# Optimization experiments

Measured on AMD Instinct MI355X. Metric: run time of the kernel, lower is better.

## Reference

```python
import jax, jax.numpy as jnp
import numpy as np

N, D = 131072, 64
VOCAB = 1_000_000
N_NEG = 1024
TEMPERATURE = 1.0
EPS = 1e-10
NEG_FILL = -1e9


def setup_inputs() -> dict:
    key = jax.random.key(0)
    k1, k2, k3, k4, k5 = jax.random.split(key, 5)
    hidden = jax.random.normal(k1, (N, D), dtype=jnp.float32)
    y = jax.random.randint(k2, (N,), 0, VOCAB, dtype=jnp.int64)
    sampled_indices = jax.random.randint(k3, (N_NEG,), 0, VOCAB, dtype=jnp.int64)
    emb_table = jax.random.normal(k4, (VOCAB, D), dtype=jnp.float32) * 0.02
    p = jax.random.uniform(k5, (VOCAB,), dtype=jnp.float32) + EPS
    sampling_probs = p / p.sum()  # normalized popularity distribution (buffer)
    return {"hidden": hidden, "y": y, "sampled_indices": sampled_indices,
            "emb_table": emb_table, "sampling_probs": sampling_probs}


def reference(hidden, y, sampled_indices, emb_table, sampling_probs):
    # torch masks rows with y == 0 before the loss; we use weighted mean instead
    # (identical math, jit-friendly static shapes).
    mask = (y != 0).astype(hidden.dtype)                      # [N]
    e_pos = emb_table[y]                                      # [N, D] gather
    e_neg = emb_table[sampled_indices]                        # [K, D] gather
    pos_logits = jnp.einsum('nd,nd->n', hidden, e_pos)        # [N]
    neg_logits = hidden @ e_neg.T                             # [N, K]
    collision = y[:, None] == sampled_indices[None, :]        # [N, K]
    neg_logits = jnp.where(collision, NEG_FILL, neg_logits)
    true_probs = sampling_probs[y]                            # [N]
    sample_probs = sampling_probs[sampled_indices]            # [K]
    pos = pos_logits / TEMPERATURE - jnp.log(true_probs + EPS)        # [N]
    neg = neg_logits / TEMPERATURE - jnp.log(sample_probs + EPS)[None, :]
    logits = jnp.concatenate([pos[:, None], neg], axis=1)     # [N, 1+K]
    # cross-entropy with label 0: logsumexp - logits[:, 0]
    ce = jax.nn.logsumexp(logits, axis=-1) - logits[:, 0]     # [N]
    return jnp.sum(ce * mask) / jnp.maximum(jnp.sum(mask), 1.0)
```

## Files before the change

kernel.cpp:

```cpp
#include <hip/hip_runtime.h>

#define N_ROWS 131072
#define DIM 64
#define KNEG 1024
#define FEPS 1e-10f
#define LOG2E 1.4426950408889634f
#define HSLOTS 2048
#define CPI 128
#define OUTER (KNEG / CPI)
#define CSTR 72

typedef __attribute__((ext_vector_type(8))) short bf16x8;
typedef __attribute__((ext_vector_type(4))) float f32x4;

__device__ __forceinline__ unsigned short f2bf(float x) {
    unsigned int u = __float_as_uint(x);
    unsigned int r = (u + 0x7fffu + ((u >> 16) & 1u)) >> 16;
    return (unsigned short)r;
}

#if __has_builtin(__builtin_amdgcn_exp2f)
__device__ __forceinline__ float fexp2(float x) { return __builtin_amdgcn_exp2f(x); }
#else
__device__ __forceinline__ float fexp2(float x) {
    float r; asm("v_exp_f32 %0, %1\ns_nop 1" : "=v"(r) : "v"(x)); return r;
}
#endif

__device__ __forceinline__ bf16x8 cvt8(float4 u, float4 v) {
    bf16x8 r;
    r[0] = (short)f2bf(u.x * LOG2E); r[1] = (short)f2bf(u.y * LOG2E);
    r[2] = (short)f2bf(u.z * LOG2E); r[3] = (short)f2bf(u.w * LOG2E);
    r[4] = (short)f2bf(v.x * LOG2E); r[5] = (short)f2bf(v.y * LOG2E);
    r[6] = (short)f2bf(v.z * LOG2E); r[7] = (short)f2bf(v.w * LOG2E);
    return r;
}

__global__ __launch_bounds__(1024) void prep_k(
    const float* __restrict__ emb, const int* __restrict__ sidx,
    const float* __restrict__ probs,
    unsigned short* __restrict__ enegPK, float* __restrict__ lf,
    float* __restrict__ gv, int* __restrict__ hkey, float* __restrict__ hval)
{
    const int tid = threadIdx.x;
    if (blockIdx.x < 16) {
        const int gid = blockIdx.x * 1024 + tid;
        const int col = gid >> 4;
        const int j   = gid & 15;
        const int c = sidx[col];
        const float4 v = *(const float4*)(emb + (size_t)c * DIM + j * 4);
        unsigned int lo = (unsigned int)f2bf(v.x) | ((unsigned int)f2bf(v.y) << 16);
        unsigned int hi = (unsigned int)f2bf(v.z) | ((unsigned int)f2bf(v.w) << 16);
        ((uint2*)enegPK)[(size_t)col * 16 + j] = make_uint2(lo, hi);
    } else {
        for (int s = tid; s < HSLOTS; s += 1024) { hkey[s] = -1; hval[s] = 0.0f; }
        const int c = sidx[tid];
        const float L = logf(probs[c] + FEPS);
        __shared__ float red[1024];
        red[tid] = -L;
        __syncthreads();
        for (int s2 = 512; s2 > 0; s2 >>= 1) {
            if (tid < s2) red[tid] = fmaxf(red[tid], red[tid + s2]);
            __syncthreads();
        }
        const float G = red[0] + 2.0f;
        if (tid == 0) gv[0] = G;
        const float lfv = (-L - G) * LOG2E;
        lf[tid] = lfv;
        const float fc = exp2f(lfv);
        unsigned int slot = ((unsigned int)c * 2654435761u) & (HSLOTS - 1);
        for (int it = 0; it < HSLOTS; ++it) {
            int old = atomicCAS(&hkey[slot], -1, c);
            if (old == -1 || old == c) { atomicAdd(&hval[slot], fc); break; }
            slot = (slot + 1) & (HSLOTS - 1);
        }
    }
}

__global__ __launch_bounds__(256, 4) void main_k(
    const float* __restrict__ hidden, const int* __restrict__ y,
    const float* __restrict__ emb, const float* __restrict__ probs,
    const unsigned short* __restrict__ enegPK, const float* __restrict__ lf,
    const float* __restrict__ gv, const int* __restrict__ hkey,
    const float* __restrict__ hval,
    float* __restrict__ pv, float* __restrict__ pw)
{
    __shared__ __align__(16) short bt[2][CPI * CSTR];
    __shared__ float lf_lds[KNEG];

    const int tid  = threadIdx.x;
    const int wid  = tid >> 6;
    const int lane = tid & 63;
    const int quad = lane >> 4;
    const int l15  = lane & 15;

    const int row0 = (blockIdx.x * 4 + wid) * 32;
    const int r0 = row0 + l15;
    const int r1 = row0 + 16 + l15;

    const int y0 = y[r0];
    const int y1 = y[r1];

    for (int i = tid; i < KNEG; i += 256) lf_lds[i] = lf[i];

    const uint4* g4 = (const uint4*)enegPK;
    const int cw = tid >> 3;
    const int ow = tid & 7;
    {
        uint4 u0 = g4[tid], u1 = g4[tid + 256], u2 = g4[tid + 512], u3 = g4[tid + 768];
        short* dst = &bt[0][0];
        *((uint4*)(dst + (cw +  0) * CSTR) + ow) = u0;
        *((uint4*)(dst + (cw + 32) * CSTR) + ow) = u1;
        *((uint4*)(dst + (cw + 64) * CSTR) + ow) = u2;
        *((uint4*)(dst + (cw + 96) * CSTR) + ow) = u3;
    }

    const float* hp0 = hidden + (size_t)r0 * DIM + quad * 8;
    const float* hp1 = hidden + (size_t)r1 * DIM + quad * 8;
    const float4 a0 = *(const float4*)(hp0 + 0);
    const float4 a1 = *(const float4*)(hp0 + 4);
    const float4 a2 = *(const float4*)(hp0 + 32);
    const float4 a3 = *(const float4*)(hp0 + 36);
    const float4 c0 = *(const float4*)(hp1 + 0);
    const float4 c1 = *(const float4*)(hp1 + 4);
    const float4 c2 = *(const float4*)(hp1 + 32);
    const float4 c3 = *(const float4*)(hp1 + 36);

    const float* pe0 = emb + (size_t)y0 * DIM + quad * 8;
    const float* pe1 = emb + (size_t)y1 * DIM + quad * 8;
    const float4 e0 = *(const float4*)(pe0 + 0);
    const float4 e1 = *(const float4*)(pe0 + 4);
    const float4 e2 = *(const float4*)(pe0 + 32);
    const float4 e3 = *(const float4*)(pe0 + 36);
    const float4 g0 = *(const float4*)(pe1 + 0);
    const float4 g1 = *(const float4*)(pe1 + 4);
    const float4 g2 = *(const float4*)(pe1 + 32);
    const float4 g3 = *(const float4*)(pe1 + 36);
    float pd0 = a0.x*e0.x + a0.y*e0.y + a0.z*e0.z + a0.w*e0.w
              + a1.x*e1.x + a1.y*e1.y + a1.z*e1.z + a1.w*e1.w
              + a2.x*e2.x + a2.y*e2.y + a2.z*e2.z + a2.w*e2.w
              + a3.x*e3.x + a3.y*e3.y + a3.z*e3.z + a3.w*e3.w;
    float pd1 = c0.x*g0.x + c0.y*g0.y + c0.z*g0.z + c0.w*g0.w
              + c1.x*g1.x + c1.y*g1.y + c1.z*g1.z + c1.w*g1.w
              + c2.x*g2.x + c2.y*g2.y + c2.z*g2.z + c2.w*g2.w
              + c3.x*g3.x + c3.y*g3.y + c3.z*g3.z + c3.w*g3.w;
    pd0 += __shfl_xor(pd0, 16, 64); pd0 += __shfl_xor(pd0, 32, 64);
    pd1 += __shfl_xor(pd1, 16, 64); pd1 += __shfl_xor(pd1, 32, 64);

    const bf16x8 h00 = cvt8(a0, a1), h01 = cvt8(a2, a3);
    const bf16x8 h10 = cvt8(c0, c1), h11 = cvt8(c2, c3);

    __syncthreads();

    float s00 = 0.f, s01 = 0.f, s02 = 0.f, s03 = 0.f;
    float s10 = 0.f, s11 = 0.f, s12 = 0.f, s13 = 0.f;
    int p = 0;

    for (int t = 0; t < OUTER; ++t) {
        uint4 u0, u1, u2, u3;
        const bool has = (t + 1 < OUTER);
        if (has) {
            const uint4* gs = g4 + (t + 1) * 1024;
            u0 = gs[tid]; u1 = gs[tid + 256]; u2 = gs[tid + 512]; u3 = gs[tid + 768];
        }
#pragma unroll
        for (int tt = 0; tt < 8; ++tt) {
            const short* bp = &bt[p][(tt * 16 + l15) * CSTR + quad * 8];
            const bf16x8 b0 = *(const bf16x8*)bp;
            const bf16x8 b1 = *(const bf16x8*)(bp + 32);
            const float lfv = lf_lds[t * CPI + tt * 16 + l15];
            f32x4 acc0 = {lfv, lfv, lfv, lfv};
            acc0 = __builtin_amdgcn_mfma_f32_16x16x32_bf16(h00, b0, acc0, 0, 0, 0);
            acc0 = __builtin_amdgcn_mfma_f32_16x16x32_bf16(h01, b1, acc0, 0, 0, 0);
            f32x4 acc1 = {lfv, lfv, lfv, lfv};
            acc1 = __builtin_amdgcn_mfma_f32_16x16x32_bf16(h10, b0, acc1, 0, 0, 0);
            acc1 = __builtin_amdgcn_mfma_f32_16x16x32_bf16(h11, b1, acc1, 0, 0, 0);
            s00 += fexp2(acc0[0]); s01 += fexp2(acc0[1]);
            s02 += fexp2(acc0[2]); s03 += fexp2(acc0[3]);
            s10 += fexp2(acc1[0]); s11 += fexp2(acc1[1]);
            s12 += fexp2(acc1[2]); s13 += fexp2(acc1[3]);
        }
        __syncthreads();
        if (has) {
            short* dst = &bt[p ^ 1][0];
            *((uint4*)(dst + (cw +  0) * CSTR) + ow) = u0;
            *((uint4*)(dst + (cw + 32) * CSTR) + ow) = u1;
            *((uint4*)(dst + (cw + 64) * CSTR) + ow) = u2;
            *((uint4*)(dst + (cw + 96) * CSTR) + ow) = u3;
        }
        __syncthreads();
        p ^= 1;
    }

#pragma unroll
    for (int m = 8; m > 0; m >>= 1) {
        s00 += __shfl_xor(s00, m, 64); s01 += __shfl_xor(s01, m, 64);
        s02 += __shfl_xor(s02, m, 64); s03 += __shfl_xor(s03, m, 64);
        s10 += __shfl_xor(s10, m, 64); s11 += __shfl_xor(s11, m, 64);
        s12 += __shfl_xor(s12, m, 64); s13 += __shfl_xor(s13, m, 64);
    }
    float sa0 = (lane & 1) ? s01 : s00;
    float sb0 = (lane & 1) ? s03 : s02;
    float sv0 = (lane & 2) ? sb0 : sa0;
    sv0 = __shfl(sv0, ((l15 >> 2) << 4) + l15, 64);
    float sa1 = (lane & 1) ? s11 : s10;
    float sb1 = (lane & 1) ? s13 : s12;
    float sv1 = (lane & 2) ? sb1 : sa1;
    sv1 = __shfl(sv1, ((l15 >> 2) << 4) + l15, 64);

    const float G = gv[0];
    float v = 0.f, ww = 0.f;
    {
        const float pos = pd0 - logf(probs[y0] + FEPS);
        float H = 0.0f;
        unsigned int slot = ((unsigned int)y0 * 2654435761u) & (HSLOTS - 1);
        for (int it = 0; it < HSLOTS; ++it) {
            const int k = hkey[slot];
            if (k == y0) { H = hval[slot]; break; }
            if (k == -1) break;
            slot = (slot + 1) & (HSLOTS - 1);
        }
        float sneg = fmaxf(sv0 - exp2f(pd0 * LOG2E) * H, 0.0f);
        const float M = fmaxf(G, pos);
        const float lse = M + logf(exp2f((pos - M) * LOG2E) + sneg * exp2f((G - M) * LOG2E));
        const float w = (y0 != 0) ? 1.0f : 0.0f;
        v += (lse - pos) * w; ww += w;
    }
    {
        const float pos = pd1 - logf(probs[y1] + FEPS);
        float H = 0.0f;
        unsigned int slot = ((unsigned int)y1 * 2654435761u) & (HSLOTS - 1);
        for (int it = 0; it < HSLOTS; ++it) {
            const int k = hkey[slot];
            if (k == y1) { H = hval[slot]; break; }
            if (k == -1) break;
            slot = (slot + 1) & (HSLOTS - 1);
        }
        float sneg = fmaxf(sv1 - exp2f(pd1 * LOG2E) * H, 0.0f);
        const float M = fmaxf(G, pos);
        const float lse = M + logf(exp2f((pos - M) * LOG2E) + sneg * exp2f((G - M) * LOG2E));
        const float w = (y1 != 0) ? 1.0f : 0.0f;
        v += (lse - pos) * w; ww += w;
    }
#pragma unroll
    for (int m = 8; m > 0; m >>= 1) {
        v  += __shfl_xor(v, m, 64);
        ww += __shfl_xor(ww, m, 64);
    }
    if (lane == 0) {
        const int wgid = blockIdx.x * 4 + wid;
        pv[wgid] = v;
        pw[wgid] = ww;
    }
}

__global__ __launch_bounds__(256) void fin_k(
    const float* __restrict__ pv, const float* __restrict__ pw,
    float* __restrict__ out)
{
    const int tid = threadIdx.x;
    double av = 0.0, aw = 0.0;
    for (int i = tid; i < N_ROWS / 32; i += 256) { av += pv[i]; aw += pw[i]; }
    __shared__ double rv[256], rw[256];
    rv[tid] = av; rw[tid] = aw;
    __syncthreads();
    for (int s2 = 128; s2 > 0; s2 >>= 1) {
        if (tid < s2) { rv[tid] += rv[tid + s2]; rw[tid] += rw[tid + s2]; }
        __syncthreads();
    }
    if (tid == 0) {
        double c = rw[0] < 1.0 ? 1.0 : rw[0];
        out[0] = (float)(rv[0] / c);
    }
}

extern "C" void kernel_launch(void* const* d_in, const int* in_sizes, int n_in,
                              void* d_out, int out_size, void* d_ws, size_t ws_size,
                              hipStream_t stream) {
    const float* hidden = (const float*)d_in[0];
    const int*   yv     = (const int*)d_in[1];
    const int*   sidx   = (const int*)d_in[2];
    const float* emb    = (const float*)d_in[3];
    const float* probs  = (const float*)d_in[4];
    float* out = (float*)d_out;

    char* ws = (char*)d_ws;
    unsigned short* enegPK = (unsigned short*)(ws);
    float* lf   = (float*)(ws + 131072);
    float* gv   = (float*)(ws + 135168);
    int*   hkey = (int*)(ws + 135424);
    float* hval = (float*)(ws + 143616);
    float* pv   = (float*)(ws + 151808);
    float* pw   = (float*)(ws + 168192);

    prep_k<<<17, 1024, 0, stream>>>(emb, sidx, probs, enegPK, lf, gv, hkey, hval);
    main_k<<<N_ROWS / 128, 256, 0, stream>>>(hidden, yv, emb, probs, enegPK,
                                             lf, gv, hkey, hval, pv, pw);
    fin_k<<<1, 256, 0, stream>>>(pv, pw, out);
}
```

Baseline: 59.88 us.

## Halve LDS chunk size, drop a barrier, and reshape prep kernel to 256-thread blocks

The main kernel now stages 64 negative columns per iteration instead of 128, so each double-buffered LDS tile is smaller and more iterations run. It also drops the barrier between compute and the write to the other buffer, leaving one barrier per iteration. The prep kernel moves from 1024-thread to 256-thread blocks, with each thread of the reduction block handling four samples. Removing the barrier is safe only because double buffering keeps reads and writes on different buffers; the smaller chunk adds loop and barrier overhead.

Result: slower. 64.19 us (+7.2%).

```diff
diff --git a/kernel.cpp b/kernel.cpp
--- a/kernel.cpp
+++ b/kernel.cpp
@@ -6,7 +6,7 @@
 #define FEPS 1e-10f
 #define LOG2E 1.4426950408889634f
 #define HSLOTS 2048
-#define CPI 128
+#define CPI 64
 #define OUTER (KNEG / CPI)
 #define CSTR 72
 
@@ -36,15 +36,15 @@
     return r;
 }
 
-__global__ __launch_bounds__(1024) void prep_k(
+__global__ __launch_bounds__(256) void prep_k(
     const float* __restrict__ emb, const int* __restrict__ sidx,
     const float* __restrict__ probs,
     unsigned short* __restrict__ enegPK, float* __restrict__ lf,
     float* __restrict__ gv, int* __restrict__ hkey, float* __restrict__ hval)
 {
     const int tid = threadIdx.x;
-    if (blockIdx.x < 16) {
-        const int gid = blockIdx.x * 1024 + tid;
+    if (blockIdx.x < 64) {
+        const int gid = blockIdx.x * 256 + tid;
         const int col = gid >> 4;
         const int j   = gid & 15;
         const int c = sidx[col];
@@ -53,26 +53,36 @@
         unsigned int hi = (unsigned int)f2bf(v.z) | ((unsigned int)f2bf(v.w) << 16);
         ((uint2*)enegPK)[(size_t)col * 16 + j] = make_uint2(lo, hi);
     } else {
-        for (int s = tid; s < HSLOTS; s += 1024) { hkey[s] = -1; hval[s] = 0.0f; }
-        const int c = sidx[tid];
-        const float L = logf(probs[c] + FEPS);
-        __shared__ float red[1024];
-        red[tid] = -L;
+        for (int s = tid; s < HSLOTS; s += 256) { hkey[s] = -1; hval[s] = 0.0f; }
+        float L[4];
+        float m = -1e30f;
+        int cs[4];
+#pragma unroll
+        for (int i = 0; i < 4; ++i) {
+            cs[i] = sidx[tid * 4 + i];
+            L[i] = logf(probs[cs[i]] + FEPS);
+            m = fmaxf(m, -L[i]);
+        }
+        __shared__ float red[256];
+        red[tid] = m;
         __syncthreads();
-        for (int s2 = 512; s2 > 0; s2 >>= 1) {
+        for (int s2 = 128; s2 > 0; s2 >>= 1) {
             if (tid < s2) red[tid] = fmaxf(red[tid], red[tid + s2]);
             __syncthreads();
         }
         const float G = red[0] + 2.0f;
         if (tid == 0) gv[0] = G;
-        const float lfv = (-L - G) * LOG2E;
-        lf[tid] = lfv;
-        const float fc = exp2f(lfv);
-        unsigned int slot = ((unsigned int)c * 2654435761u) & (HSLOTS - 1);
-        for (int it = 0; it < HSLOTS; ++it) {
-            int old = atomicCAS(&hkey[slot], -1, c);
-            if (old == -1 || old == c) { atomicAdd(&hval[slot], fc); break; }
-            slot = (slot + 1) & (HSLOTS - 1);
+#pragma unroll
+        for (int i = 0; i < 4; ++i) {
+            const float lfv = (-L[i] - G) * LOG2E;
+            lf[tid * 4 + i] = lfv;
+            const float fc = exp2f(lfv);
+            unsigned int slot = ((unsigned int)cs[i] * 2654435761u) & (HSLOTS - 1);
+            for (int it = 0; it < HSLOTS; ++it) {
+                int old = atomicCAS(&hkey[slot], -1, cs[i]);
+                if (old == -1 || old == cs[i]) { atomicAdd(&hval[slot], fc); break; }
+                slot = (slot + 1) & (HSLOTS - 1);
+            }
         }
     }
 }
@@ -96,7 +106,7 @@
 
     const int row0 = (blockIdx.x * 4 + wid) * 32;
     const int r0 = row0 + l15;
-    const int r1 = row0 + 16 + l15;
+    const int r1 = r0 + 16;
 
     const int y0 = y[r0];
     const int y1 = y[r1];
@@ -104,15 +114,13 @@
     for (int i = tid; i < KNEG; i += 256) lf_lds[i] = lf[i];
 
     const uint4* g4 = (const uint4*)enegPK;
-    const int cw = tid >> 3;
-    const int ow = tid & 7;
+    const int cw0 = tid >> 3;
+    const int cw1 = (tid + 256) >> 3;
+    const int ow  = tid & 7;
     {
-        uint4 u0 = g4[tid], u1 = g4[tid + 256], u2 = g4[tid + 512], u3 = g4[tid + 768];
-        short* dst = &bt[0][0];
-        *((uint4*)(dst + (cw +  0) * CSTR) + ow) = u0;
-        *((uint4*)(dst + (cw + 32) * CSTR) + ow) = u1;
-        *((uint4*)(dst + (cw + 64) * CSTR) + ow) = u2;
-        *((uint4*)(dst + (cw + 96) * CSTR) + ow) = u3;
+        uint4 u0 = g4[tid], u1 = g4[tid + 256];
+        *((uint4*)(&bt[0][cw0 * CSTR]) + ow) = u0;
+        *((uint4*)(&bt[0][cw1 * CSTR]) + ow) = u1;
     }
 
     const float* hp0 = hidden + (size_t)r0 * DIM + quad * 8;
@@ -157,14 +165,14 @@
     int p = 0;
 
     for (int t = 0; t < OUTER; ++t) {
-        uint4 u0, u1, u2, u3;
+        uint4 u0, u1;
         const bool has = (t + 1 < OUTER);
         if (has) {
-            const uint4* gs = g4 + (t + 1) * 1024;
-            u0 = gs[tid]; u1 = gs[tid + 256]; u2 = gs[tid + 512]; u3 = gs[tid + 768];
-        }
-#pragma unroll
-        for (int tt = 0; tt < 8; ++tt) {
+            const uint4* gs = g4 + (t + 1) * 512;
+            u0 = gs[tid]; u1 = gs[tid + 256];
+        }
+#pragma unroll
+        for (int tt = 0; tt < CPI / 16; ++tt) {
             const short* bp = &bt[p][(tt * 16 + l15) * CSTR + quad * 8];
             const bf16x8 b0 = *(const bf16x8*)bp;
             const bf16x8 b1 = *(const bf16x8*)(bp + 32);
@@ -180,13 +188,9 @@
             s10 += fexp2(acc1[0]); s11 += fexp2(acc1[1]);
             s12 += fexp2(acc1[2]); s13 += fexp2(acc1[3]);
         }
-        __syncthreads();
         if (has) {
-            short* dst = &bt[p ^ 1][0];
-            *((uint4*)(dst + (cw +  0) * CSTR) + ow) = u0;
-            *((uint4*)(dst + (cw + 32) * CSTR) + ow) = u1;
-            *((uint4*)(dst + (cw + 64) * CSTR) + ow) = u2;
-            *((uint4*)(dst + (cw + 96) * CSTR) + ow) = u3;
+            *((uint4*)(&bt[p ^ 1][cw0 * CSTR]) + ow) = u0;
+            *((uint4*)(&bt[p ^ 1][cw1 * CSTR]) + ow) = u1;
         }
         __syncthreads();
         p ^= 1;
@@ -293,7 +297,7 @@
     float* pv   = (float*)(ws + 151808);
     float* pw   = (float*)(ws + 168192);
 
-    prep_k<<<17, 1024, 0, stream>>>(emb, sidx, probs, enegPK, lf, gv, hkey, hval);
+    prep_k<<<65, 256, 0, stream>>>(emb, sidx, probs, enegPK, lf, gv, hkey, hval);
     main_k<<<N_ROWS / 128, 256, 0, stream>>>(hidden, yv, emb, probs, enegPK,
                                              lf, gv, hkey, hval, pv, pw);
     fin_k<<<1, 256, 0, stream>>>(pv, pw, out);
```
